# Kernel optimization log

Measured on AMD Instinct MI355X. Metric: run time of the kernel, lower is better.

Reference implementation:

```python
import jax, jax.numpy as jnp
import numpy as np

# Model dims (see init_kwargs)
B, S, D = 2, 2048, 2048          # batch, seq, hidden
H, HD = 16, 128                  # heads, head_dim (= ND + RD)
ND, RD = 64, 64                  # nope dim, rope dim per head
R = 512                          # kv lora rank
THETA = 10000.0


def _rotate_half(x):
    # interleaved rotation: pairs (x0,x1) -> (-x1, x0)
    x1 = x[..., ::2]
    x2 = x[..., 1::2]
    return jnp.stack((-x2, x1), axis=-1).reshape(x.shape)


def apply_rope(x, positions):
    # x: [..., seq, dim]
    dim = x.shape[-1]
    freqs = 1.0 / THETA ** (jnp.arange(0, dim, 2, dtype=x.dtype) / dim)  # [dim/2]
    angles = positions.astype(x.dtype)[:, None] * freqs                  # [seq, dim/2]
    cos = jnp.repeat(jnp.cos(angles), 2, axis=-1)[None, None]            # [1,1,seq,dim]
    sin = jnp.repeat(jnp.sin(angles), 2, axis=-1)[None, None]
    return x * cos + _rotate_half(x) * sin


def setup_inputs() -> dict:
    key = jax.random.key(0)
    ks = jax.random.split(key, 7)
    def lin(k, out_f, in_f):  # torch Linear convention: weight [out, in]
        return jax.random.normal(k, (out_f, in_f), dtype=jnp.float32) * (in_f ** -0.5)
    return {
        "x": jax.random.normal(ks[0], (B, S, D), dtype=jnp.float32),
        "wq": lin(ks[1], D, D),
        "w_kv_down": lin(ks[2], R, D),
        "w_k_up": lin(ks[3], H * ND, R),
        "w_k_rope": lin(ks[4], RD, D),
        "w_v_up": lin(ks[5], D, R),
        "wo": lin(ks[6], D, D),
    }


def reference(x, wq, w_kv_down, w_k_up, w_k_rope, w_v_up, wo):
    b, s, _ = x.shape
    pos = jnp.arange(s)
    scale = 1.0 / np.sqrt(HD).astype(np.float32)

    # queries: [b,H,s,HD] split into nope/rope parts, rope applied per head
    q = (x @ wq.T).reshape(b, s, H, HD).transpose(0, 2, 1, 3)
    q_nope = q[..., :ND]
    q_rope = apply_rope(q[..., ND:], pos)

    # compressed kv latent: [b,s,R]
    c_kv = x @ w_kv_down.T
    k_nope = (c_kv @ w_k_up.T).reshape(b, s, H, ND).transpose(0, 2, 1, 3)  # [b,H,s,ND]
    k_rope = apply_rope((x @ w_k_rope.T)[:, None], pos)[:, 0]             # [b,s,RD], shared across heads
    v = (c_kv @ w_v_up.T).reshape(b, s, H, HD).transpose(0, 2, 1, 3)      # [b,H,s,HD]

    # decomposed scores: nope part (per head) + rope part (shared k)
    scores = jnp.einsum('bhqd,bhkd->bhqk', q_nope, k_nope)
    scores = scores + jnp.einsum('bhqd,bkd->bhqk', q_rope, k_rope)
    scores = scores * scale

    causal = jnp.tril(jnp.ones((s, s), dtype=bool))
    scores = jnp.where(causal[None, None], scores, jnp.finfo(scores.dtype).min)
    attn = jax.nn.softmax(scores, axis=-1)

    out = jnp.einsum('bhqk,bhkd->bhqd', attn, v)
    out = out.transpose(0, 2, 1, 3).reshape(b, s, D)
    return out @ wo.T
```

## Files before the change

### kernel.cpp

```cpp
#include <hip/hip_runtime.h>
#include <stdint.h>


typedef unsigned short u16;
typedef __bf16 bf16x8 __attribute__((ext_vector_type(8)));
typedef float f32x4 __attribute__((ext_vector_type(4)));

__device__ __forceinline__ float bf2f(u16 u) {
    union { unsigned int i; float f; } x; x.i = ((unsigned int)u) << 16; return x.f;
}
__device__ __forceinline__ u16 f2bf(float f) {
    union { float f; unsigned int i; } x; x.f = f;
    unsigned int r = x.i + 0x7fffu + ((x.i >> 16) & 1u);
    return (u16)(r >> 16);
}
__device__ __forceinline__ void store_c(u16* p, float v)  { *p = f2bf(v); }
__device__ __forceinline__ void store_c(float* p, float v){ *p = v; }

#define GLOBAL_AS __attribute__((address_space(1)))
#define LDS_AS    __attribute__((address_space(3)))
__device__ __forceinline__ void gl_lds16(const void* g, void* l) {
    __builtin_amdgcn_global_load_lds((GLOBAL_AS const void*)g, (LDS_AS void*)l, 16, 0, 0);
}

#if __has_builtin(__builtin_amdgcn_exp2f)
__device__ __forceinline__ float exp2fast(float x) { return __builtin_amdgcn_exp2f(x); }
#else
__device__ __forceinline__ float exp2fast(float x) { return __expf(x * 0.6931471805599453f); }
#endif

template<int CTRL>
__device__ __forceinline__ float fmax_dpp(float v) {
    int s = __builtin_bit_cast(int, v);
    int t = __builtin_amdgcn_update_dpp(s, s, CTRL, 0xF, 0xF, true);
    return fmaxf(v, __builtin_bit_cast(float, t));
}
__device__ __forceinline__ float rowmax16(float v) {
    v = fmax_dpp<0xB1>(v);
    v = fmax_dpp<0x4E>(v);
    v = fmax_dpp<0x124>(v);
    v = fmax_dpp<0x128>(v);
    return v;
}

__global__ void convert_in(const float* __restrict__ src, u16* __restrict__ dst,
                           int n8) {
    int i = blockIdx.x * 256 + threadIdx.x;
    if (i >= n8) return;
    const float4* s = (const float4*)src;
    float4 v0 = s[2*i], v1 = s[2*i + 1];
    union { u16 u[8]; uint4 v; } o;
    o.u[0] = f2bf(v0.x); o.u[1] = f2bf(v0.y); o.u[2] = f2bf(v0.z); o.u[3] = f2bf(v0.w);
    o.u[4] = f2bf(v1.x); o.u[5] = f2bf(v1.y); o.u[6] = f2bf(v1.z); o.u[7] = f2bf(v1.w);
    *((uint4*)(dst + 8*i)) = o.v;
}

template<int BM, int BN, int EPI, typename CT>
__global__ __launch_bounds__((BM/64)*(BN/64)*64)
void gemm_bt(const u16* __restrict__ A, const u16* __restrict__ W,
             CT* __restrict__ C, int M, int N, int K,
             int lda, int ldw, int ldc) {
    constexpr int BK = 32;
    constexpr int NWAVE = (BM/64)*(BN/64);
    constexpr int NT = NWAVE * 64;
    __shared__ u16 As[BM*BK];
    __shared__ u16 Bs[BN*BK];
    const int tid  = threadIdx.x;
    const int lane = tid & 63, l15 = lane & 15, quad = lane >> 4;
    const int wave = tid >> 6;
    const int wm = wave % (BM/64);
    const int wn = wave / (BM/64);
    const int bm = blockIdx.y * BM;
    const int bn = blockIdx.x * BN;

    const f32x4 fzero = {0.f, 0.f, 0.f, 0.f};
    f32x4 acc[4][4];
    #pragma unroll
    for (int i = 0; i < 4; ++i)
        #pragma unroll
        for (int j = 0; j < 4; ++j) acc[i][j] = fzero;

    const size_t Ab = (size_t)lda * 2;
    const size_t Wb = (size_t)ldw * 2;

    for (int k0 = 0; k0 < K; k0 += BK) {
        #pragma unroll
        for (int i = 0; i < (BM*64)/(NT*16); ++i) {
            int o = (tid + i*NT) * 16;
            int row = o >> 6, colb = o & 63;
            gl_lds16((const char*)A + (size_t)(bm + row)*Ab + (size_t)k0*2 + colb,
                     (char*)As + o);
        }
        #pragma unroll
        for (int i = 0; i < (BN*64)/(NT*16); ++i) {
            int o = (tid + i*NT) * 16;
            int row = o >> 6, colb = o & 63;
            gl_lds16((const char*)W + (size_t)(bn + row)*Wb + (size_t)k0*2 + colb,
                     (char*)Bs + o);
        }
        __syncthreads();

        bf16x8 af[4], bfv[4];
        #pragma unroll
        for (int mt = 0; mt < 4; ++mt)
            af[mt] = *reinterpret_cast<const bf16x8*>(&As[(wm*64 + mt*16 + l15)*BK + quad*8]);
        #pragma unroll
        for (int nt = 0; nt < 4; ++nt)
            bfv[nt] = *reinterpret_cast<const bf16x8*>(&Bs[(wn*64 + nt*16 + l15)*BK + quad*8]);
        #pragma unroll
        for (int mt = 0; mt < 4; ++mt)
            #pragma unroll
            for (int nt = 0; nt < 4; ++nt)
                acc[mt][nt] = __builtin_amdgcn_mfma_f32_16x16x32_bf16(
                    af[mt], bfv[nt], acc[mt][nt], 0, 0, 0);
        __syncthreads();
    }

    #pragma unroll
    for (int mt = 0; mt < 4; ++mt)
        #pragma unroll
        for (int nt = 0; nt < 4; ++nt)
            #pragma unroll
            for (int r = 0; r < 4; ++r) {
                int gm = bm + wm*64 + mt*16 + quad*4 + r;
                int gn = bn + wn*64 + nt*16 + l15;
                size_t ci;
                if (EPI == 1) ci = (size_t)gm*ldc + ((gn >> 6)*128 + (gn & 63));
                else          ci = (size_t)gm*ldc + gn;
                store_c(&C[ci], acc[mt][nt][r]);
            }
}

__global__ void rope_q(u16* __restrict__ qcat) {
    int idx = blockIdx.x * 256 + threadIdx.x;
    int i = idx & 31, r = idx >> 5;
    int pos = r & 2047;
    float freq = powf(10000.0f, -(float)i * (1.0f/32.0f));
    float ang  = (float)pos * freq;
    float s = sinf(ang), c = cosf(ang);
    u16* row = qcat + (size_t)r * 2688 + 64 + 2*i;
    #pragma unroll
    for (int h = 0; h < 16; ++h) {
        unsigned int* p = (unsigned int*)(row + h*128);
        unsigned int v = *p;
        float x0 = bf2f((u16)(v & 0xffffu)), x1 = bf2f((u16)(v >> 16));
        unsigned int lo = f2bf(x0*c - x1*s);
        unsigned int hi = f2bf(x1*c + x0*s);
        *p = lo | (hi << 16);
    }
}

__global__ void rope_kr_bcast(const u16* __restrict__ qcat, u16* __restrict__ keff) {
    int idx = blockIdx.x * 256 + threadIdx.x;
    int i = idx & 31, r = idx >> 5;
    int pos = r & 2047;
    float freq = powf(10000.0f, -(float)i * (1.0f/32.0f));
    float ang  = (float)pos * freq;
    float s = sinf(ang), c = cosf(ang);
    const u16* p = qcat + (size_t)r * 2688 + 2048 + 2*i;
    float x0 = bf2f(p[0]), x1 = bf2f(p[1]);
    union { u16 u[2]; unsigned int w; } o;
    o.u[0] = f2bf(x0*c - x1*s);
    o.u[1] = f2bf(x1*c + x0*s);
    unsigned int* base = (unsigned int*)(keff + (size_t)r*2048 + 64 + 2*i);
    #pragma unroll
    for (int h = 0; h < 16; ++h) base[h*64] = o.w;
}

__global__ __launch_bounds__(256, 3)
void attn_kernel(u16* __restrict__ qcat, const u16* __restrict__ KE,
                 const u16* __restrict__ VT) {
    constexpr int S = 2048;
    const int L = (int)blockIdx.y * 16 + (int)blockIdx.x;
    const int xcd = L & 7, j = L >> 3;
    const int bh   = xcd * 4 + (j & 3);
    const int pair = j >> 2;
    const int b = bh >> 4, h = bh & 15;

    __shared__ u16 Ks[64*128];
    __shared__ u16 Vs[128*64];
    __shared__ u16 Ps[64*68];

    const int tid  = threadIdx.x;
    const int lane = tid & 63, l15 = lane & 15, quad = lane >> 4;
    const int wave = tid >> 6;

    const u16* ksrc[4];
    const u16* vsrc[4];
    #pragma unroll
    for (int i = 0; i < 4; ++i) {
        int g = tid + i*256;
        {
            int r = g >> 4, slot = g & 15, cg = slot ^ (r & 15);
            ksrc[i] = KE + (size_t)(b*S + r)*2048 + h*128 + cg*8;
        }
        {
            int d = g >> 3, slot = g & 7, cg = slot ^ (d & 7);
            vsrc[i] = VT + (size_t)(h*128 + d)*4096 + (size_t)(b*S) + cg*8;
        }
    }

    bf16x8 kreg[4], vreg[4];
    #pragma unroll
    for (int i = 0; i < 4; ++i) {
        kreg[i] = *reinterpret_cast<const bf16x8*>(ksrc[i]);
        vreg[i] = *reinterpret_cast<const bf16x8*>(vsrc[i]);
    }

    union { u16 u[8]; bf16x8 v; } onesu;
    #pragma unroll
    for (int i = 0; i < 8; ++i) onesu.u[i] = 0x3f80;
    const bf16x8 ones = onesu.v;

    const f32x4 fzero = {0.f, 0.f, 0.f, 0.f};
    const float NEG = -1e30f;
    const float KLOG = 0.12751739f;
    const float THR = 8.0f;

    __bf16* PsB = reinterpret_cast<__bf16*>(Ps);

    for (int half = 0; half < 2; ++half) {
        const int qt = half ? pair : 31 - pair;
        const int nkt = qt + 1;

        u16* qbase = qcat + (size_t)(b*S + qt*64) * 2688 + h*128;
        bf16x8 aq[4];
        #pragma unroll
        for (int ks = 0; ks < 4; ++ks)
            aq[ks] = *reinterpret_cast<const bf16x8*>(
                qbase + (size_t)(wave*16 + l15)*2688 + ks*32 + quad*8);

        float m2[4]  = {NEG, NEG, NEG, NEG};
        float l_i[4] = {0.f, 0.f, 0.f, 0.f};
        f32x4 oacc[8];
        #pragma unroll
        for (int i = 0; i < 8; ++i) oacc[i] = fzero;

        const int qrow0 = qt*64 + wave*16 + quad*4;

        for (int kt = 0; kt < nkt; ++kt) {
            const bool is_last = (kt == nkt - 1);
            #pragma unroll
            for (int i = 0; i < 4; ++i) {
                *reinterpret_cast<bf16x8*>(&Ks[(tid + i*256) * 8]) = kreg[i];
                *reinterpret_cast<bf16x8*>(&Vs[(tid + i*256) * 8]) = vreg[i];
            }
            {
                int ktn = (kt + 1 < nkt) ? kt + 1 : 0;
                #pragma unroll
                for (int i = 0; i < 4; ++i) {
                    kreg[i] = *reinterpret_cast<const bf16x8*>(ksrc[i] + (size_t)ktn*(64*2048));
                    vreg[i] = *reinterpret_cast<const bf16x8*>(vsrc[i] + (size_t)ktn*64);
                }
            }
            __syncthreads();

            f32x4 sfr[4];
            #pragma unroll
            for (int nt = 0; nt < 4; ++nt) {
                f32x4 s = fzero;
                int n = nt*16 + l15;
                #pragma unroll
                for (int ks = 0; ks < 4; ++ks) {
                    int c = ks*4 + quad;
                    bf16x8 bk = *reinterpret_cast<const bf16x8*>(&Ks[n*128 + ((c ^ l15) * 8)]);
                    s = __builtin_amdgcn_mfma_f32_16x16x32_bf16(aq[ks], bk, s, 0, 0, 0);
                }
                sfr[nt] = s;
            }
            if (is_last) {
                #pragma unroll
                for (int nt = 0; nt < 4; ++nt) {
                    int kg = kt*64 + nt*16 + l15;
                    #pragma unroll
                    for (int r = 0; r < 4; ++r)
                        if (kg > qrow0 + r) sfr[nt][r] = NEG;
                }
            }
            float rm[4];
            #pragma unroll
            for (int r = 0; r < 4; ++r) {
                rm[r] = fmaxf(fmaxf(sfr[0][r], sfr[1][r]), fmaxf(sfr[2][r], sfr[3][r]));
                rm[r] = rowmax16(rm[r]);
            }
            float c2[4];
            int need = 0;
            #pragma unroll
            for (int r = 0; r < 4; ++r) {
                c2[r] = rm[r] * KLOG;
                need |= (c2[r] > m2[r] + THR) ? 1 : 0;
            }
            if (__any(need)) {
                float alpha[4];
                #pragma unroll
                for (int r = 0; r < 4; ++r) {
                    float mn = fmaxf(m2[r], c2[r]);
                    alpha[r] = exp2fast(m2[r] - mn);
                    m2[r] = mn;
                    l_i[r] *= alpha[r];
                }
                #pragma unroll
                for (int i = 0; i < 8; ++i)
                    #pragma unroll
                    for (int r = 0; r < 4; ++r)
                        oacc[i][r] *= alpha[r];
            }
            float pf[4][4];
            #pragma unroll
            for (int nt = 0; nt < 4; ++nt)
                #pragma unroll
                for (int r = 0; r < 4; ++r)
                    pf[nt][r] = exp2fast(__builtin_fmaf(sfr[nt][r], KLOG, -m2[r]));

            #pragma unroll
            for (int nt = 0; nt < 4; ++nt) {
                int base = (wave*16 + quad*4)*68 + nt*16 + l15;
                #pragma unroll
                for (int r = 0; r < 4; ++r)
                    PsB[base + r*68] = (__bf16)pf[nt][r];
            }

            f32x4 lfr = fzero;
            #pragma unroll
            for (int ks = 0; ks < 2; ++ks) {
                bf16x8 pa = *reinterpret_cast<const bf16x8*>(
                    &Ps[(wave*16 + l15)*68 + ks*32 + quad*8]);
                lfr = __builtin_amdgcn_mfma_f32_16x16x32_bf16(pa, ones, lfr, 0, 0, 0);
                #pragma unroll
                for (int ntv = 0; ntv < 8; ++ntv) {
                    int c = ks*4 + quad;
                    bf16x8 bv = *reinterpret_cast<const bf16x8*>(
                        &Vs[(ntv*16 + l15)*64 + ((c ^ (l15 & 7)) * 8)]);
                    oacc[ntv] = __builtin_amdgcn_mfma_f32_16x16x32_bf16(pa, bv, oacc[ntv], 0, 0, 0);
                }
            }
            #pragma unroll
            for (int r = 0; r < 4; ++r) l_i[r] += lfr[r];
            __syncthreads();
        }

        #pragma unroll
        for (int r = 0; r < 4; ++r) {
            float inv = 1.0f / l_i[r];
            int qrow = wave*16 + quad*4 + r;
            #pragma unroll
            for (int ntv = 0; ntv < 8; ++ntv) {
                int d = ntv*16 + l15;
                qbase[(size_t)qrow*2688 + d] = f2bf(oacc[ntv][r] * inv);
            }
        }
    }
}

extern "C" void kernel_launch(void* const* d_in, const int* in_sizes, int n_in,
                              void* d_out, int out_size, void* d_ws, size_t ws_size,
                              hipStream_t stream) {
    (void)in_sizes; (void)n_in; (void)out_size; (void)ws_size;
    float* out = (float*)d_out;
    char* ws = (char*)d_ws;

    u16* xc     = (u16*)(ws);
    u16* qcat   = (u16*)(ws + 16777216);
    u16* keff   = (u16*)(ws + 38797312);
    u16* wqcat  = (u16*)(ws + 55574528);
    u16* kupc   = (u16*)(ws + 66584576);
    u16* vupc   = (u16*)(ws + 67633152);
    u16* vT     = xc;
    u16* woc    = wqcat;

    convert_in<<<(1048576+255)/256, 256, 0, stream>>>((const float*)d_in[0], xc, 1048576);
    convert_in<<<( 524288+255)/256, 256, 0, stream>>>((const float*)d_in[1], wqcat, 524288);
    convert_in<<<(  16384+255)/256, 256, 0, stream>>>((const float*)d_in[4], wqcat + 2048*2048, 16384);
    convert_in<<<( 131072+255)/256, 256, 0, stream>>>((const float*)d_in[2], wqcat + 2112*2048, 131072);
    convert_in<<<(  65536+255)/256, 256, 0, stream>>>((const float*)d_in[3], kupc, 65536);
    convert_in<<<( 131072+255)/256, 256, 0, stream>>>((const float*)d_in[5], vupc, 131072);

    gemm_bt<128,128,0><<<dim3(21, 32), 256, 0, stream>>>(
        xc, wqcat, qcat, 4096, 2688, 2048, 2048, 2048, 2688);

    convert_in<<<(524288+255)/256, 256, 0, stream>>>((const float*)d_in[6], woc, 524288);

    rope_q<<<512, 256, 0, stream>>>(qcat);
    rope_kr_bcast<<<512, 256, 0, stream>>>(qcat, keff);

    gemm_bt<128,128,1><<<dim3(8, 32), 256, 0, stream>>>(
        qcat + 2112, kupc, keff, 4096, 1024, 512, 2688, 512, 2048);

    gemm_bt<128,128,0><<<dim3(32, 16), 256, 0, stream>>>(
        vupc, qcat + 2112, vT, 2048, 4096, 512, 512, 2688, 4096);

    attn_kernel<<<dim3(16, 32), 256, 0, stream>>>(qcat, keff, vT);

    gemm_bt<128,128,0><<<dim3(16, 32), 256, 0, stream>>>(
        qcat, woc, out, 4096, 2048, 2048, 2688, 2048, 2048);
}
```

Before: 360.9 us.

## Add 256x256 multi-stage LDS-pipelined GEMM for projection and output GEMMs

Introduces a 512-thread GEMM kernel with 256x256 output tiles. It uses a 4-buffer global_load_lds pipeline with swizzled LDS reads and raised priority around the MFMA block. This kernel replaces the 128x128 GEMM for the fused Q/KV-down projection, the V-up projection and the output projection, aiming for more data reuse per tile and better overlap of loads with compute. To fit the 256-wide tiles, the qcat row stride is padded from 2688 to 2816 and the workspace offsets are shifted. The padded columns compute on whatever lies past the weight rows, and the larger tiles lower the block count and occupancy.

Result: faster. 347.1 us (-3.8%).

```diff
diff --git a/kernel.cpp b/kernel.cpp
--- a/kernel.cpp
+++ b/kernel.cpp
@@ -5,6 +5,8 @@
 typedef unsigned short u16;
 typedef __bf16 bf16x8 __attribute__((ext_vector_type(8)));
 typedef float f32x4 __attribute__((ext_vector_type(4)));
+
+#define QLD 2816
 
 __device__ __forceinline__ float bf2f(u16 u) {
     union { unsigned int i; float f; } x; x.i = ((unsigned int)u) << 16; return x.f;
@@ -131,6 +133,90 @@
             }
 }
 
+template<typename CT>
+__global__ __launch_bounds__(512, 2)
+void gemm256(const u16* __restrict__ A, const u16* __restrict__ W,
+             CT* __restrict__ C, int K, int lda, int ldw, int ldc) {
+    __shared__ u16 lds[4][16384];
+    const int tid  = threadIdx.x;
+    const int lane = tid & 63, l15 = lane & 15, quad = lane >> 4;
+    const int wave = tid >> 6;
+    const int wr = wave >> 2, wc = wave & 3;
+    const int bm = blockIdx.y * 256;
+    const int bn = blockIdx.x * 256;
+
+    const int R = tid >> 2, slot = tid & 3;
+    const int k16 = slot ^ ((R >> 1) & 3);
+    const u16* asrc = A + (size_t)(bm + R) * lda + k16 * 8;
+    const u16* bsrc = W + (size_t)(bn + R) * ldw + k16 * 8;
+    const size_t astep = (size_t)128 * lda;
+    const size_t bstep = (size_t)128 * ldw;
+
+    #define STAGE256(st, bi) { \
+        const u16* a0_ = asrc + (size_t)(st) * 32; \
+        const u16* b0_ = bsrc + (size_t)(st) * 32; \
+        gl_lds16(a0_,         &lds[bi][tid * 8]); \
+        gl_lds16(a0_ + astep, &lds[bi][(tid + 512) * 8]); \
+        gl_lds16(b0_,         &lds[bi][(tid + 1024) * 8]); \
+        gl_lds16(b0_ + bstep, &lds[bi][(tid + 1536) * 8]); \
+    }
+
+    const f32x4 fzero = {0.f, 0.f, 0.f, 0.f};
+    f32x4 acc[8][4];
+    #pragma unroll
+    for (int i = 0; i < 8; ++i)
+        #pragma unroll
+        for (int j = 0; j < 4; ++j) acc[i][j] = fzero;
+
+    const int aswz = (quad ^ ((l15 >> 1) & 3)) * 8;
+
+    const int nst = K >> 5;
+    STAGE256(0, 0)
+    STAGE256(1, 1)
+    STAGE256(2, 2)
+    asm volatile("s_waitcnt vmcnt(8)" ::: "memory");
+    __builtin_amdgcn_s_barrier();
+
+    for (int t = 0; t < nst; ++t) {
+        const u16* buf = lds[t & 3];
+        bf16x8 af[8], bfv[4];
+        #pragma unroll
+        for (int mf = 0; mf < 8; ++mf)
+            af[mf] = *reinterpret_cast<const bf16x8*>(
+                &buf[(wr*128 + mf*16 + l15)*32 + aswz]);
+        #pragma unroll
+        for (int nf = 0; nf < 4; ++nf)
+            bfv[nf] = *reinterpret_cast<const bf16x8*>(
+                &buf[8192 + (wc*64 + nf*16 + l15)*32 + aswz]);
+        int st = t + 3; if (st > nst - 1) st = nst - 1;
+        STAGE256(st, (t + 3) & 3)
+        __builtin_amdgcn_s_setprio(1);
+        #pragma unroll
+        for (int mf = 0; mf < 8; ++mf)
+            #pragma unroll
+            for (int nf = 0; nf < 4; ++nf)
+                acc[mf][nf] = __builtin_amdgcn_mfma_f32_16x16x32_bf16(
+                    af[mf], bfv[nf], acc[mf][nf], 0, 0, 0);
+        __builtin_amdgcn_s_setprio(0);
+        asm volatile("s_waitcnt vmcnt(8) lgkmcnt(0)" ::: "memory");
+        __builtin_amdgcn_sched_barrier(0);
+        __builtin_amdgcn_s_barrier();
+        __builtin_amdgcn_sched_barrier(0);
+    }
+    #undef STAGE256
+
+    #pragma unroll
+    for (int mf = 0; mf < 8; ++mf)
+        #pragma unroll
+        for (int nf = 0; nf < 4; ++nf)
+            #pragma unroll
+            for (int r = 0; r < 4; ++r) {
+                int gm = bm + wr*128 + mf*16 + quad*4 + r;
+                int gn = bn + wc*64 + nf*16 + l15;
+                store_c(&C[(size_t)gm * ldc + gn], acc[mf][nf][r]);
+            }
+}
+
 __global__ void rope_q(u16* __restrict__ qcat) {
     int idx = blockIdx.x * 256 + threadIdx.x;
     int i = idx & 31, r = idx >> 5;
@@ -138,7 +224,7 @@
     float freq = powf(10000.0f, -(float)i * (1.0f/32.0f));
     float ang  = (float)pos * freq;
     float s = sinf(ang), c = cosf(ang);
-    u16* row = qcat + (size_t)r * 2688 + 64 + 2*i;
+    u16* row = qcat + (size_t)r * QLD + 64 + 2*i;
     #pragma unroll
     for (int h = 0; h < 16; ++h) {
         unsigned int* p = (unsigned int*)(row + h*128);
@@ -157,7 +243,7 @@
     float freq = powf(10000.0f, -(float)i * (1.0f/32.0f));
     float ang  = (float)pos * freq;
     float s = sinf(ang), c = cosf(ang);
-    const u16* p = qcat + (size_t)r * 2688 + 2048 + 2*i;
+    const u16* p = qcat + (size_t)r * QLD + 2048 + 2*i;
     float x0 = bf2f(p[0]), x1 = bf2f(p[1]);
     union { u16 u[2]; unsigned int w; } o;
     o.u[0] = f2bf(x0*c - x1*s);
@@ -223,12 +309,12 @@
         const int qt = half ? pair : 31 - pair;
         const int nkt = qt + 1;
 
-        u16* qbase = qcat + (size_t)(b*S + qt*64) * 2688 + h*128;
+        u16* qbase = qcat + (size_t)(b*S + qt*64) * QLD + h*128;
         bf16x8 aq[4];
         #pragma unroll
         for (int ks = 0; ks < 4; ++ks)
             aq[ks] = *reinterpret_cast<const bf16x8*>(
-                qbase + (size_t)(wave*16 + l15)*2688 + ks*32 + quad*8);
+                qbase + (size_t)(wave*16 + l15)*QLD + ks*32 + quad*8);
 
         float m2[4]  = {NEG, NEG, NEG, NEG};
         float l_i[4] = {0.f, 0.f, 0.f, 0.f};
@@ -346,7 +432,7 @@
             #pragma unroll
             for (int ntv = 0; ntv < 8; ++ntv) {
                 int d = ntv*16 + l15;
-                qbase[(size_t)qrow*2688 + d] = f2bf(oacc[ntv][r] * inv);
+                qbase[(size_t)qrow*QLD + d] = f2bf(oacc[ntv][r] * inv);
             }
         }
     }
@@ -361,10 +447,10 @@
 
     u16* xc     = (u16*)(ws);
     u16* qcat   = (u16*)(ws + 16777216);
-    u16* keff   = (u16*)(ws + 38797312);
-    u16* wqcat  = (u16*)(ws + 55574528);
-    u16* kupc   = (u16*)(ws + 66584576);
-    u16* vupc   = (u16*)(ws + 67633152);
+    u16* keff   = (u16*)(ws + 39845888);
+    u16* wqcat  = (u16*)(ws + 56623104);
+    u16* kupc   = (u16*)(ws + 68157440);
+    u16* vupc   = (u16*)(ws + 69206016);
     u16* vT     = xc;
     u16* woc    = wqcat;
 
@@ -375,8 +461,8 @@
     convert_in<<<(  65536+255)/256, 256, 0, stream>>>((const float*)d_in[3], kupc, 65536);
     convert_in<<<( 131072+255)/256, 256, 0, stream>>>((const float*)d_in[5], vupc, 131072);
 
-    gemm_bt<128,128,0><<<dim3(21, 32), 256, 0, stream>>>(
-        xc, wqcat, qcat, 4096, 2688, 2048, 2048, 2048, 2688);
+    gemm256<u16><<<dim3(11, 16), 512, 0, stream>>>(
+        xc, wqcat, qcat, 2048, 2048, 2048, QLD);
 
     convert_in<<<(524288+255)/256, 256, 0, stream>>>((const float*)d_in[6], woc, 524288);
 
@@ -384,13 +470,13 @@
     rope_kr_bcast<<<512, 256, 0, stream>>>(qcat, keff);
 
     gemm_bt<128,128,1><<<dim3(8, 32), 256, 0, stream>>>(
-        qcat + 2112, kupc, keff, 4096, 1024, 512, 2688, 512, 2048);
-
-    gemm_bt<128,128,0><<<dim3(32, 16), 256, 0, stream>>>(
-        vupc, qcat + 2112, vT, 2048, 4096, 512, 512, 2688, 4096);
+        qcat + 2112, kupc, keff, 4096, 1024, 512, QLD, 512, 2048);
+
+    gemm256<u16><<<dim3(16, 8), 512, 0, stream>>>(
+        vupc, qcat + 2112, vT, 512, 512, QLD, 4096);
 
     attn_kernel<<<dim3(16, 32), 256, 0, stream>>>(qcat, keff, vT);
 
-    gemm_bt<128,128,0><<<dim3(16, 32), 256, 0, stream>>>(
-        qcat, woc, out, 4096, 2048, 2048, 2688, 2048, 2048);
-}
+    gemm256<float><<<dim3(8, 16), 512, 0, stream>>>(
+        qcat, woc, out, 2048, QLD, 2048, 2048);
+}
```
